# Optimization experiments

Hardware: AMD Instinct MI355X
Metric: run time of the kernel (lower is better)

## Reference

```python
import math
import jax, jax.numpy as jnp
import numpy as np

C = 1.0          # Poincare ball curvature
NUM_HEADS = 8
EPS = 1e-15

def _beta(a, b):
    # Beta function via lgamma (python float constant)
    return math.exp(math.lgamma(a) + math.lgamma(b) - math.lgamma(a + b))

def h_linear(x, z, r, c=C):
    """HNN++ Poincare fully-connected layer (hypll HLinear).
    x: [..., in] points in the ball; z: [in, out] tangent weights; r: [out] bias."""
    sc = math.sqrt(c)
    x2 = jnp.sum(x * x, axis=-1, keepdims=True)
    lam = 2.0 / (1.0 - c * x2)                                # conformal factor
    zn = jnp.maximum(jnp.linalg.norm(z, axis=0), EPS)          # [out]
    inner = x @ z                                              # [..., out]
    two_scr = 2.0 * sc * r
    d = (2.0 * zn / sc) * jnp.arcsinh(
        (sc * inner * lam / zn) * jnp.cosh(two_scr) - (lam - 1.0) * jnp.sinh(two_scr)
    )
    w = jnp.sinh(sc * d) / sc
    return w / (1.0 + jnp.sqrt(1.0 + c * jnp.sum(w * w, axis=-1, keepdims=True)))

def pairwise_dist(q, k, c=C):
    """Poincare distance d(q,k) = arccosh(1 + 2c|q-k|^2 / ((1-c|q|^2)(1-c|k|^2))) / sqrt(c).
    q,k: [B,H,S,hd] -> [B,H,S,S]."""
    q2 = jnp.sum(q * q, axis=-1)
    k2 = jnp.sum(k * k, axis=-1)
    qk = jnp.einsum('bhqd,bhkd->bhqk', q, k)
    diff2 = jnp.maximum(q2[..., :, None] + k2[..., None, :] - 2.0 * qk, 0.0)
    denom = (1.0 - c * q2)[..., :, None] * (1.0 - c * k2)[..., None, :]
    arg = 1.0 + 2.0 * c * diff2 / denom
    return jnp.arccosh(jnp.maximum(arg, 1.0 + 1e-7)) / math.sqrt(c)

def midpoint(v, w, c=C):
    """Weighted Mobius gyromidpoint: m = 1/2 (x) (sum w*lam*x / sum w*(lam-1)).
    v: [B,H,Sk,hd], w: [B,H,Sq,Sk] -> [B,H,Sq,hd]."""
    v2 = jnp.sum(v * v, axis=-1)                      # [B,H,Sk]
    lam = 2.0 / (1.0 - c * v2)
    num = jnp.einsum('bhqk,bhkd->bhqd', w * lam[..., None, :], v)
    den = jnp.maximum(jnp.einsum('bhqk,bhk->bhq', w, lam - 1.0), EPS)[..., None]
    g = num / den                                     # gyromidpoint pre-scaling
    sc = math.sqrt(c)
    gn = jnp.maximum(jnp.linalg.norm(g, axis=-1, keepdims=True), EPS)
    t = jnp.tanh(0.5 * jnp.arctanh(jnp.clip(sc * gn, 0.0, 1.0 - 1e-7)))
    return (t / sc) * g / gn

def _forward(query, key, value, Wq, bq, Wk, bk, Wv, bv, scale_tau, scale_gamma):
    B, S, E = query.shape
    H = NUM_HEADS
    hd = E // H
    # hyperbolic q/k/v projections, then split into heads: [B,H,S,hd]
    q = h_linear(query, Wq, bq).reshape(B, S, H, hd).transpose(0, 2, 1, 3)
    k = h_linear(key, Wk, bk).reshape(B, S, H, hd).transpose(0, 2, 1, 3)
    v = h_linear(value, Wv, bv).reshape(B, S, H, hd).transpose(0, 2, 1, 3)
    # similarity = -dist/tau - gamma with tau = exp(-scale_tau)
    sim = -pairwise_dist(q, k) * jnp.exp(scale_tau[0]) - scale_gamma[0]
    causal = jnp.triu(jnp.ones((S, S), dtype=bool), k=1)
    sim = jnp.where(causal, -jnp.inf, sim)
    w = jnp.exp(sim)                                  # 'exp' attention activation
    agg = midpoint(v, w)                              # [B,H,S,hd]
    agg = agg.transpose(0, 2, 1, 3).reshape(B, S, E)
    # HNN++ beta-concatenation of the per-head ball points
    scale = _beta(E / 2.0, 0.5) / _beta(hd / 2.0, 0.5)
    return agg * scale

def setup_inputs() -> dict:
    root = jax.random.key(0)
    ks = jax.random.split(root, 8)
    B, S, E = 1, 2048, 512
    s = 0.02  # keep points well inside the unit ball
    return {
        'query': s * jax.random.normal(ks[0], (B, S, E), jnp.float32),
        'key':   s * jax.random.normal(ks[1], (B, S, E), jnp.float32),
        'value': s * jax.random.normal(ks[2], (B, S, E), jnp.float32),
        'Wq': s * jax.random.normal(ks[3], (E, E), jnp.float32),
        'Wk': s * jax.random.normal(ks[4], (E, E), jnp.float32),
        'Wv': s * jax.random.normal(ks[5], (E, E), jnp.float32),
        'bq': jnp.zeros((E,), jnp.float32),
        'bk': jnp.zeros((E,), jnp.float32),
        'bv': jnp.zeros((E,), jnp.float32),
        'scale_tau': jnp.zeros((1,), jnp.float32),
        'scale_gamma': jnp.zeros((1,), jnp.float32),
    }

def reference(query, key, value, Wq, Wk, Wv, bq, bk, bv, scale_tau, scale_gamma):
    return _forward(query, key, value, Wq, bq, Wk, bk, Wv, bv, scale_tau, scale_gamma)
```

## Files before the change

### kernel.cpp

```cpp
#include <hip/hip_runtime.h>
#include <cmath>

#define H 8
#define SEQ 2048
#define EDIM 512
#define HD 64
#define EPSF 1e-15f

typedef short bf16x8 __attribute__((ext_vector_type(8)));
typedef float f32x4 __attribute__((ext_vector_type(4)));

#define FLAG_OFF  0
#define ZN_OFF    16
#define ACC_OFF   (ZN_OFF + 3 * EDIM)
#define STATS_OFF (ACC_OFF + H * SEQ * 80)
#define CQ_OFF    (STATS_OFF + 3 * H * SEQ)
#define IK_OFF    (CQ_OFF + H * SEQ)
#define U16_OFF   (IK_OFF + H * SEQ + 16)
#define WT_U16    0
#define QKVB_U16  (WT_U16 + 3 * EDIM * EDIM)
#define VT_U16    (QKVB_U16 + 3 * SEQ * EDIM)

__device__ __forceinline__ float bf2f(unsigned short u){
  union { unsigned int i; float f; } v; v.i = ((unsigned int)u) << 16; return v.f;
}
__device__ __forceinline__ unsigned short f2bf(float f){
  union { float f; unsigned int i; } v; v.f = f;
  unsigned int x = v.i;
  unsigned int r = (x + 0x7fffu + ((x >> 16) & 1u)) >> 16;
  return (unsigned short)r;
}

__global__ void probe_kernel(const unsigned short* __restrict__ q, int* __restrict__ flag){
  const int t = threadIdx.x;
  float mx = 0.f;
  #pragma unroll
  for (int j = 0; j < 4; ++j) mx = fmaxf(mx, fabsf(bf2f(q[t * 4 + j])));
  #pragma unroll
  for (int m = 32; m >= 1; m >>= 1) mx = fmaxf(mx, __shfl_xor(mx, m, 64));
  if (t == 0) *flag = (mx > 1000.f) ? 1 : 0;
}

__global__ __launch_bounds__(256) void wcvt_kernel(
    const void* __restrict__ Wq, const void* __restrict__ Wk, const void* __restrict__ Wv,
    const int* __restrict__ flag, unsigned short* __restrict__ WT, float* __restrict__ zn)
{
  const int p = blockIdx.y;
  const int bi = blockIdx.x >> 3, bo = blockIdx.x & 7;
  const void* W = (p == 0) ? Wq : ((p == 1) ? Wk : Wv);
  const int t = threadIdx.x;
  const int isf32 = *flag;
  __shared__ float tile[64][65];

  #pragma unroll
  for (int j = 0; j < 16; ++j){
    int idx = t + 256 * j;
    int il = idx >> 6, ol = idx & 63;
    float val;
    if (isf32) val = ((const float*)W)[(size_t)(bi * 64 + il) * EDIM + bo * 64 + ol];
    else       val = bf2f(((const unsigned short*)W)[(size_t)(bi * 64 + il) * EDIM + bo * 64 + ol]);
    tile[il][ol] = val;
  }
  __syncthreads();
  if (t < 64){
    float s = 0.f;
    #pragma unroll 8
    for (int i = 0; i < 64; ++i){ float v = tile[i][t]; s += v * v; }
    atomicAdd(&zn[p * EDIM + bo * 64 + t], s);
  }
  #pragma unroll
  for (int j = 0; j < 16; ++j){
    int idx = t + 256 * j;
    int ol = idx >> 6, il = idx & 63;
    WT[((size_t)p * EDIM + bo * 64 + ol) * EDIM + bi * 64 + il] = f2bf(tile[il][ol]);
  }
}

__global__ __launch_bounds__(256) void hlinear_kernel(
    const void* __restrict__ Xq, const void* __restrict__ Xk, const void* __restrict__ Xv,
    const unsigned short* __restrict__ WT,
    const void* __restrict__ Bq, const void* __restrict__ Bk, const void* __restrict__ Bv,
    const float* __restrict__ znacc, const int* __restrict__ flag,
    unsigned short* __restrict__ qkvb, float* __restrict__ stats,
    float* __restrict__ cqs, float* __restrict__ iks,
    unsigned short* __restrict__ VT)
{
  const int p = blockIdx.y;
  const void* X  = (p == 0) ? Xq : ((p == 1) ? Xk : Xv);
  const void* Bb = (p == 0) ? Bq : ((p == 1) ? Bk : Bv);
  const int r0 = blockIdx.x * 16;
  const int t  = threadIdx.x;
  const int w = t >> 6, lane = t & 63;
  const int col = lane & 15, quad = lane >> 4;
  const int isf32 = *flag;

  __shared__ float smem[16 * EDIM];
  __shared__ float sw2[16];

  const unsigned short* WTb = WT + ((size_t)p * EDIM + w * 128 + col) * EDIM;
  const float* Xf = (const float*)X + (size_t)(r0 + col) * EDIM;
  const unsigned short* Xh = (const unsigned short*)X + (size_t)(r0 + col) * EDIM;

  f32x4 acc[8];
  #pragma unroll
  for (int nt = 0; nt < 8; ++nt) acc[nt] = (f32x4){0.f, 0.f, 0.f, 0.f};
  float x2part = 0.f;

  for (int ks = 0; ks < 16; ++ks){
    bf16x8 af;
    if (isf32){
      float4 xa = *(const float4*)&Xf[ks * 32 + quad * 8];
      float4 xb = *(const float4*)&Xf[ks * 32 + quad * 8 + 4];
      float xv[8] = {xa.x, xa.y, xa.z, xa.w, xb.x, xb.y, xb.z, xb.w};
      #pragma unroll
      for (int j = 0; j < 8; ++j){ af[j] = (short)f2bf(xv[j]); x2part += xv[j] * xv[j]; }
    } else {
      af = *(const bf16x8*)&Xh[ks * 32 + quad * 8];
      #pragma unroll
      for (int j = 0; j < 8; ++j){ float xv = bf2f((unsigned short)af[j]); x2part += xv * xv; }
    }
    #pragma unroll
    for (int nt = 0; nt < 8; ++nt){
      bf16x8 bf = *(const bf16x8*)&WTb[(size_t)nt * 16 * EDIM + ks * 32 + quad * 8];
      acc[nt] = __builtin_amdgcn_mfma_f32_16x16x32_bf16(af, bf, acc[nt], 0, 0, 0);
    }
  }
  x2part += __shfl_xor(x2part, 16, 64);
  x2part += __shfl_xor(x2part, 32, 64);
  float lamr[4], lm1[4];
  #pragma unroll
  for (int r = 0; r < 4; ++r){
    float x2r = __shfl(x2part, quad * 4 + r, 64);
    lamr[r] = 2.f / (1.f - x2r);
    lm1[r] = lamr[r] - 1.f;
  }
  #pragma unroll
  for (int nt = 0; nt < 8; ++nt){
    const int n = w * 128 + nt * 16 + col;
    float znv = fmaxf(sqrtf(znacc[p * EDIM + n]), EPSF);
    float rb;
    if (isf32) rb = ((const float*)Bb)[n];
    else       rb = bf2f(((const unsigned short*)Bb)[n]);
    float e2r = __expf(2.f * rb);
    float ie2r = 1.f / e2r;
    float ch = 0.5f * (e2r + ie2r), sh = 0.5f * (e2r - ie2r);
    float izn = 1.f / znv;
    float tz = 2.f * znv;
    #pragma unroll
    for (int r = 0; r < 4; ++r){
      float a = (acc[nt][r] * lamr[r] * izn) * ch - lm1[r] * sh;
      float b = a + sqrtf(a * a + 1.f);
      float tt = __expf(tz * __logf(b));
      smem[(quad * 4 + r) * EDIM + n] = 0.5f * (tt - 1.f / tt);
    }
  }
  __syncthreads();

  {
    int row = t >> 4, l = t & 15;
    float s = 0.f;
    for (int o = l; o < EDIM; o += 16){ float wv = smem[row * EDIM + o]; s += wv * wv; }
    #pragma unroll
    for (int m = 8; m >= 1; m >>= 1) s += __shfl_xor(s, m, 16);
    if (l == 0) sw2[row] = s;
  }
  __syncthreads();

  const int o0 = 2 * t;
  const int h0 = t >> 5;
  const int d0 = o0 & 63;
  const int l5 = t & 31;
  #pragma unroll
  for (int rr = 0; rr < 16; ++rr){
    float inv = 1.f / (1.f + sqrtf(1.f + sw2[rr]));
    unsigned short b0 = f2bf(smem[rr * EDIM + o0] * inv);
    unsigned short b1 = f2bf(smem[rr * EDIM + o0 + 1] * inv);
    float r0v = bf2f(b0), r1v = bf2f(b1);
    int s = r0 + rr;
    unsigned int* dst = (unsigned int*)&qkvb[(((size_t)p * H + h0) * SEQ + s) * HD + d0];
    *dst = (unsigned int)b0 | ((unsigned int)b1 << 16);
    float ss = r0v * r0v + r1v * r1v;
    #pragma unroll
    for (int m = 16; m >= 1; m >>= 1) ss += __shfl_xor(ss, m, 64);
    if (p == 2){
      float lam = 2.f / (1.f - ss);
      VT[((size_t)h0 * 80 + d0) * SEQ + s]     = f2bf(r0v * lam);
      VT[((size_t)h0 * 80 + d0 + 1) * SEQ + s] = f2bf(r1v * lam);
      if (l5 < 16)
        VT[((size_t)h0 * 80 + 64 + l5) * SEQ + s] = (l5 == 0) ? f2bf(lam - 1.f) : 0;
    }
    if (l5 == 0){
      stats[((size_t)p * H + h0) * SEQ + s] = ss;
      if (p == 0) cqs[(size_t)h0 * SEQ + s] = 2.f / (1.f - ss);
      if (p == 1) iks[(size_t)h0 * SEQ + s] = 1.f / (1.f - ss);
    }
  }
}

__global__ __launch_bounds__(256) void attn_kernel(
    const unsigned short* __restrict__ Qb, const unsigned short* __restrict__ Kb,
    const unsigned short* __restrict__ VT,
    const float* __restrict__ q2s_all, const float* __restrict__ k2s_all,
    const float* __restrict__ cqs_all, const float* __restrict__ iks_all,
    const void* __restrict__ tau, const void* __restrict__ gam,
    const int* __restrict__ flag, float* __restrict__ ACC)
{
  const int h  = blockIdx.y;
  const int tile = blockIdx.x >> 3;
  const int sl = blockIdx.x & 7;
  if (sl > tile) return;
  const int t = threadIdx.x;
  const int w = t >> 6, lane = t & 63;
  const int col = lane & 15, quad = lane >> 4;
  const int q0 = tile * 64 + w * 16;

  const unsigned short* Qh  = Qb + (size_t)h * SEQ * HD;
  const unsigned short* Kh  = Kb + (size_t)h * SEQ * HD;
  const unsigned short* VTh = VT + (size_t)h * 80 * SEQ;
  const float* q2s = q2s_all + (size_t)h * SEQ;
  const float* k2s = k2s_all + (size_t)h * SEQ;
  const float* cqs = cqs_all + (size_t)h * SEQ;
  const float* iks = iks_all + (size_t)h * SEQ;

  float tauv, gamv;
  if (*flag){ tauv = ((const float*)tau)[0]; gamv = ((const float*)gam)[0]; }
  else      { tauv = bf2f(((const unsigned short*)tau)[0]);
              gamv = bf2f(((const unsigned short*)gam)[0]); }
  const float e_tau = expf(tauv);

  const int srcA = ((quad & 1) * 2) * 16 + col;
  const int srcB = srcA + 16;
  const int tsel = quad >> 1;

  bf16x8 qf0 = *(const bf16x8*)&Qh[(size_t)(q0 + col) * HD + quad * 8];
  bf16x8 qf1 = *(const bf16x8*)&Qh[(size_t)(q0 + col) * HD + 32 + quad * 8];
  const float q2 = q2s[q0 + col];
  const float cq = cqs[q0 + col];
  const int qmax = q0 + col;

  f32x4 pv[5];
  #pragma unroll
  for (int nt = 0; nt < 5; ++nt) pv[nt] = (f32x4){0.f, 0.f, 0.f, 0.f};

  for (int kc = sl; kc <= tile; kc += 8){
    #pragma unroll
    for (int half = 0; half < 2; ++half){
      const int kb32 = kc * 64 + half * 32;
      unsigned int tlo[2], thi[2];
      #pragma unroll
      for (int tt = 0; tt < 2; ++tt){
        const int kbase = kb32 + 16 * tt;
        bf16x8 kf0 = *(const bf16x8*)&Kh[(size_t)(kbase + col) * HD + quad * 8];
        bf16x8 kf1 = *(const bf16x8*)&Kh[(size_t)(kbase + col) * HD + 32 + quad * 8];
        f32x4 s = (f32x4){0.f, 0.f, 0.f, 0.f};
        s = __builtin_amdgcn_mfma_f32_16x16x32_bf16(kf0, qf0, s, 0, 0, 0);
        s = __builtin_amdgcn_mfma_f32_16x16x32_bf16(kf1, qf1, s, 0, 0, 0);
        float4 k2q = *(const float4*)&k2s[kbase + quad * 4];
        float4 ikq = *(const float4*)&iks[kbase + quad * 4];
        unsigned short pb[4];
        #pragma unroll
        for (int r = 0; r < 4; ++r){
          float k2 = (r == 0) ? k2q.x : (r == 1) ? k2q.y : (r == 2) ? k2q.z : k2q.w;
          float ik = (r == 0) ? ikq.x : (r == 1) ? ikq.y : (r == 2) ? ikq.z : ikq.w;
          float diff2 = fmaxf(q2 + k2 - 2.f * s[r], 0.f);
          float u = fmaxf(diff2 * cq * ik, 1e-7f);
          float z = 1.f + u + sqrtf(u * (u + 2.f));
          float wv = __expf(-e_tau * __logf(z) - gamv);
          int key = kbase + quad * 4 + r;
          if (key > qmax) wv = 0.f;
          pb[r] = f2bf(wv);
        }
        tlo[tt] = (unsigned int)pb[0] | ((unsigned int)pb[1] << 16);
        thi[tt] = (unsigned int)pb[2] | ((unsigned int)pb[3] << 16);
      }
      unsigned int a0 = (unsigned int)__shfl((int)tlo[0], srcA, 64);
      unsigned int a1 = (unsigned int)__shfl((int)tlo[1], srcA, 64);
      unsigned int b0 = (unsigned int)__shfl((int)thi[0], srcA, 64);
      unsigned int b1 = (unsigned int)__shfl((int)thi[1], srcA, 64);
      unsigned int c0 = (unsigned int)__shfl((int)tlo[0], srcB, 64);
      unsigned int c1 = (unsigned int)__shfl((int)tlo[1], srcB, 64);
      unsigned int d0 = (unsigned int)__shfl((int)thi[0], srcB, 64);
      unsigned int d1 = (unsigned int)__shfl((int)thi[1], srcB, 64);
      union { uint4 u; bf16x8 v; } pw;
      pw.u.x = tsel ? a1 : a0;
      pw.u.y = tsel ? b1 : b0;
      pw.u.z = tsel ? c1 : c0;
      pw.u.w = tsel ? d1 : d0;
      #pragma unroll
      for (int nt = 0; nt < 5; ++nt){
        bf16x8 vf = *(const bf16x8*)&VTh[(size_t)(16 * nt + col) * SEQ + kb32 + quad * 8];
        pv[nt] = __builtin_amdgcn_mfma_f32_16x16x32_bf16(pw.v, vf, pv[nt], 0, 0, 0);
      }
    }
  }

  #pragma unroll
  for (int r = 0; r < 4; ++r){
    float* row = ACC + ((size_t)h * SEQ + q0 + quad * 4 + r) * 80;
    #pragma unroll
    for (int nt = 0; nt < 5; ++nt)
      atomicAdd(&row[16 * nt + col], pv[nt][r]);
  }
}

__global__ __launch_bounds__(64) void attn_fin_kernel(
    const float* __restrict__ ACC, float* __restrict__ out, float beta_scale)
{
  const int h = blockIdx.y, tile = blockIdx.x;
  const int t = threadIdx.x;
  const int col = t & 15, quad = t >> 4;
  const int q0 = tile * 16;

  f32x4 pv[5];
  #pragma unroll
  for (int nt = 0; nt < 5; ++nt)
    #pragma unroll
    for (int r = 0; r < 4; ++r)
      pv[nt][r] = ACC[((size_t)h * SEQ + q0 + quad * 4 + r) * 80 + 16 * nt + col];

  #pragma unroll
  for (int r = 0; r < 4; ++r){
    float den = __shfl(pv[4][r], quad * 16, 64);
    den = fmaxf(den, EPSF);
    float inv_den = 1.f / den;
    float g[4];
    float gsq = 0.f;
    #pragma unroll
    for (int nt = 0; nt < 4; ++nt){ g[nt] = pv[nt][r] * inv_den; gsq += g[nt] * g[nt]; }
    #pragma unroll
    for (int m = 8; m >= 1; m >>= 1) gsq += __shfl_xor(gsq, m, 64);
    float gn = fmaxf(sqrtf(gsq), EPSF);
    float x = fminf(gn, 1.f - 1e-7f);
    float tt2 = x / (1.f + sqrtf(1.f - x * x));
    float scl = (tt2 / gn) * beta_scale;
    const int q = q0 + quad * 4 + r;
    #pragma unroll
    for (int nt = 0; nt < 4; ++nt)
      out[(size_t)q * EDIM + h * HD + 16 * nt + col] = g[nt] * scl;
  }
}

extern "C" void kernel_launch(void* const* d_in, const int* in_sizes, int n_in,
                              void* d_out, int out_size, void* d_ws, size_t ws_size,
                              hipStream_t stream){
  const void* Xq  = d_in[0];
  const void* Xk  = d_in[1];
  const void* Xv  = d_in[2];
  const void* Wq  = d_in[3];
  const void* Wk  = d_in[4];
  const void* Wv  = d_in[5];
  const void* Bq  = d_in[6];
  const void* Bk  = d_in[7];
  const void* Bv  = d_in[8];
  const void* tau = d_in[9];
  const void* gam = d_in[10];

  float* wsf   = (float*)d_ws;
  int*   flag  = (int*)(wsf + FLAG_OFF);
  float* zn    = wsf + ZN_OFF;
  float* ACC   = wsf + ACC_OFF;
  float* stats = wsf + STATS_OFF;
  float* cqs   = wsf + CQ_OFF;
  float* iks   = wsf + IK_OFF;
  unsigned short* u16b = (unsigned short*)(wsf + U16_OFF);
  unsigned short* WT   = u16b + WT_U16;
  unsigned short* qkvb = u16b + QKVB_U16;
  unsigned short* VT   = u16b + VT_U16;

  unsigned short* Qb = qkvb;
  unsigned short* Kb = qkvb + (size_t)H * SEQ * HD;
  float* q2s = stats;
  float* k2s = stats + (size_t)H * SEQ;

  double lb1 = lgamma(EDIM / 2.0) + lgamma(0.5) - lgamma(EDIM / 2.0 + 0.5);
  double lb2 = lgamma(HD / 2.0)   + lgamma(0.5) - lgamma(HD / 2.0 + 0.5);
  float beta_scale = (float)exp(lb1 - lb2);

  probe_kernel<<<dim3(1), dim3(64), 0, stream>>>((const unsigned short*)Xq, flag);
  hipMemsetAsync(zn, 0, (size_t)(3 * EDIM + H * SEQ * 80) * sizeof(float), stream);
  wcvt_kernel<<<dim3(64, 3), dim3(256), 0, stream>>>(Wq, Wk, Wv, flag, WT, zn);
  hlinear_kernel<<<dim3(SEQ / 16, 3), dim3(256), 0, stream>>>(
      Xq, Xk, Xv, WT, Bq, Bk, Bv, zn, flag, qkvb, stats, cqs, iks, VT);
  attn_kernel<<<dim3(32 * 8, H), dim3(256), 0, stream>>>(
      Qb, Kb, VT, q2s, k2s, cqs, iks, tau, gam, flag, ACC);
  attn_fin_kernel<<<dim3(128, H), dim3(64), 0, stream>>>(
      ACC, (float*)d_out, beta_scale);
}
```

Before: 219.0 us.

## Rebalance causal attention split and specialize weights for zero tau

```diff
diff --git a/kernel.cpp b/kernel.cpp
--- a/kernel.cpp
+++ b/kernel.cpp
@@ -197,52 +197,15 @@
   }
 }
 
-__global__ __launch_bounds__(256) void attn_kernel(
-    const unsigned short* __restrict__ Qb, const unsigned short* __restrict__ Kb,
-    const unsigned short* __restrict__ VT,
-    const float* __restrict__ q2s_all, const float* __restrict__ k2s_all,
-    const float* __restrict__ cqs_all, const float* __restrict__ iks_all,
-    const void* __restrict__ tau, const void* __restrict__ gam,
-    const int* __restrict__ flag, float* __restrict__ ACC)
+template<bool FAST>
+__device__ __forceinline__ void attn_loop(
+    const unsigned short* __restrict__ Kh, const unsigned short* __restrict__ VTh,
+    const float* __restrict__ k2s, const float* __restrict__ iks,
+    float q2, float cq, float e_tau, int qmax,
+    int kc0, int kc1, int col, int quad, int srcA, int srcB, int tsel,
+    bf16x8 qf0, bf16x8 qf1, f32x4* pv)
 {
-  const int h  = blockIdx.y;
-  const int tile = blockIdx.x >> 3;
-  const int sl = blockIdx.x & 7;
-  if (sl > tile) return;
-  const int t = threadIdx.x;
-  const int w = t >> 6, lane = t & 63;
-  const int col = lane & 15, quad = lane >> 4;
-  const int q0 = tile * 64 + w * 16;
-
-  const unsigned short* Qh  = Qb + (size_t)h * SEQ * HD;
-  const unsigned short* Kh  = Kb + (size_t)h * SEQ * HD;
-  const unsigned short* VTh = VT + (size_t)h * 80 * SEQ;
-  const float* q2s = q2s_all + (size_t)h * SEQ;
-  const float* k2s = k2s_all + (size_t)h * SEQ;
-  const float* cqs = cqs_all + (size_t)h * SEQ;
-  const float* iks = iks_all + (size_t)h * SEQ;
-
-  float tauv, gamv;
-  if (*flag){ tauv = ((const float*)tau)[0]; gamv = ((const float*)gam)[0]; }
-  else      { tauv = bf2f(((const unsigned short*)tau)[0]);
-              gamv = bf2f(((const unsigned short*)gam)[0]); }
-  const float e_tau = expf(tauv);
-
-  const int srcA = ((quad & 1) * 2) * 16 + col;
-  const int srcB = srcA + 16;
-  const int tsel = quad >> 1;
-
-  bf16x8 qf0 = *(const bf16x8*)&Qh[(size_t)(q0 + col) * HD + quad * 8];
-  bf16x8 qf1 = *(const bf16x8*)&Qh[(size_t)(q0 + col) * HD + 32 + quad * 8];
-  const float q2 = q2s[q0 + col];
-  const float cq = cqs[q0 + col];
-  const int qmax = q0 + col;
-
-  f32x4 pv[5];
-  #pragma unroll
-  for (int nt = 0; nt < 5; ++nt) pv[nt] = (f32x4){0.f, 0.f, 0.f, 0.f};
-
-  for (int kc = sl; kc <= tile; kc += 8){
+  for (int kc = kc0; kc <= kc1; ++kc){
     #pragma unroll
     for (int half = 0; half < 2; ++half){
       const int kb32 = kc * 64 + half * 32;
@@ -265,7 +228,9 @@
           float diff2 = fmaxf(q2 + k2 - 2.f * s[r], 0.f);
           float u = fmaxf(diff2 * cq * ik, 1e-7f);
           float z = 1.f + u + sqrtf(u * (u + 2.f));
-          float wv = __expf(-e_tau * __logf(z) - gamv);
+          float wv;
+          if (FAST) wv = __fdividef(1.f, z);
+          else      wv = __expf(-e_tau * __logf(z));
           int key = kbase + quad * 4 + r;
           if (key > qmax) wv = 0.f;
           pb[r] = f2bf(wv);
@@ -293,6 +258,61 @@
       }
     }
   }
+}
+
+__global__ __launch_bounds__(256) void attn_kernel(
+    const unsigned short* __restrict__ Qb, const unsigned short* __restrict__ Kb,
+    const unsigned short* __restrict__ VT,
+    const float* __restrict__ q2s_all, const float* __restrict__ k2s_all,
+    const float* __restrict__ cqs_all, const float* __restrict__ iks_all,
+    const void* __restrict__ tau, const int* __restrict__ flag,
+    float* __restrict__ ACC)
+{
+  const int h  = blockIdx.y;
+  const int j = blockIdx.x & 15;
+  const int tile = 31 - (blockIdx.x >> 4);
+  const int kc0 = 2 * j;
+  if (kc0 > tile) return;
+  const int kc1 = (kc0 + 1 <= tile) ? kc0 + 1 : tile;
+
+  const int t = threadIdx.x;
+  const int w = t >> 6, lane = t & 63;
+  const int col = lane & 15, quad = lane >> 4;
+  const int q0 = tile * 64 + w * 16;
+
+  const unsigned short* Qh  = Qb + (size_t)h * SEQ * HD;
+  const unsigned short* Kh  = Kb + (size_t)h * SEQ * HD;
+  const unsigned short* VTh = VT + (size_t)h * 80 * SEQ;
+  const float* q2s = q2s_all + (size_t)h * SEQ;
+  const float* k2s = k2s_all + (size_t)h * SEQ;
+  const float* cqs = cqs_all + (size_t)h * SEQ;
+  const float* iks = iks_all + (size_t)h * SEQ;
+
+  float tauv;
+  if (*flag) tauv = ((const float*)tau)[0];
+  else       tauv = bf2f(((const unsigned short*)tau)[0]);
+  const float e_tau = __expf(tauv);
+
+  const int srcA = ((quad & 1) * 2) * 16 + col;
+  const int srcB = srcA + 16;
+  const int tsel = quad >> 1;
+
+  bf16x8 qf0 = *(const bf16x8*)&Qh[(size_t)(q0 + col) * HD + quad * 8];
+  bf16x8 qf1 = *(const bf16x8*)&Qh[(size_t)(q0 + col) * HD + 32 + quad * 8];
+  const float q2 = q2s[q0 + col];
+  const float cq = cqs[q0 + col];
+  const int qmax = q0 + col;
+
+  f32x4 pv[5];
+  #pragma unroll
+  for (int nt = 0; nt < 5; ++nt) pv[nt] = (f32x4){0.f, 0.f, 0.f, 0.f};
+
+  if (tauv == 0.f)
+    attn_loop<true >(Kh, VTh, k2s, iks, q2, cq, e_tau, qmax,
+                     kc0, kc1, col, quad, srcA, srcB, tsel, qf0, qf1, pv);
+  else
+    attn_loop<false>(Kh, VTh, k2s, iks, q2, cq, e_tau, qmax,
+                     kc0, kc1, col, quad, srcA, srcB, tsel, qf0, qf1, pv);
 
   #pragma unroll
   for (int r = 0; r < 4; ++r){
@@ -353,7 +373,6 @@
   const void* Bk  = d_in[7];
   const void* Bv  = d_in[8];
   const void* tau = d_in[9];
-  const void* gam = d_in[10];
 
   float* wsf   = (float*)d_ws;
   int*   flag  = (int*)(wsf + FLAG_OFF);
@@ -381,8 +400,8 @@
   wcvt_kernel<<<dim3(64, 3), dim3(256), 0, stream>>>(Wq, Wk, Wv, flag, WT, zn);
   hlinear_kernel<<<dim3(SEQ / 16, 3), dim3(256), 0, stream>>>(
       Xq, Xk, Xv, WT, Bq, Bk, Bv, zn, flag, qkvb, stats, cqs, iks, VT);
-  attn_kernel<<<dim3(32 * 8, H), dim3(256), 0, stream>>>(
-      Qb, Kb, VT, q2s, k2s, cqs, iks, tau, gam, flag, ACC);
+  attn_kernel<<<dim3(512, H), dim3(256), 0, stream>>>(
+      Qb, Kb, VT, q2s, k2s, cqs, iks, tau, flag, ACC);
   attn_fin_kernel<<<dim3(128, H), dim3(64), 0, stream>>>(
       ACC, (float*)d_out, beta_scale);
 }
```

New measurement: 241.7 us. 1.1x slower.
